# Kernel optimization log

Measured on AMD Instinct MI355X. Metric: run time of the kernel, lower is better.

## Reference

```python
import jax, jax.numpy as jnp
import numpy as np

RADIUS = 1.0
NSAMPLE = 32


def _query_ball(new_xyz, xyz, radius, nsample):
    # new_xyz (B,M,3), xyz (B,N,3) -> idx (B,M,nsample) int32
    B, M, _ = new_xyz.shape
    N = xyz.shape[1]
    # squared distances via ||q||^2 + ||p||^2 - 2 q.p (avoids BxMxNx3 diff tensor)
    q2 = jnp.sum(new_xyz * new_xyz, axis=-1)          # (B,M)
    p2 = jnp.sum(xyz * xyz, axis=-1)                  # (B,N)
    qp = jnp.einsum('bmd,bnd->bmn', new_xyz, xyz)     # (B,M,N)
    dist2 = q2[:, :, None] + p2[:, None, :] - 2.0 * qp
    mask = dist2 < radius * radius
    ar = jnp.arange(N, dtype=jnp.int32)
    masked = jnp.where(mask, ar[None, None, :], jnp.int32(N + 1))  # (B,M,N)
    first = jnp.sort(masked, axis=2)[:, :, :nsample]               # (B,M,S)
    first_valid = first[:, :, :1]                                   # pad with first neighbor
    idx = jnp.where(first == N + 1, first_valid, first)
    return idx.astype(jnp.int32)


def _group(points, idx):
    # points (B,C,N), idx (B,M,S) -> (B,C,M,S) gather along N
    B, C, N = points.shape
    M, S = idx.shape[1], idx.shape[2]
    ie = jnp.broadcast_to(idx.reshape(B, 1, M * S).astype(jnp.int32), (B, C, M * S))
    return jnp.take_along_axis(points, ie, axis=2).reshape(B, C, M, S)


def setup_inputs() -> dict:
    key = jax.random.key(0)
    k1, k2 = jax.random.split(key)
    B, N, M, C = 8, 8192, 2048, 64
    xyz = jax.random.normal(k1, (B, N, 3), dtype=jnp.float32)
    # centroids are a subset of the cloud -> every ball query has >= 1 valid neighbor
    new_xyz = xyz[:, :M, :]
    features = jax.random.normal(k2, (B, C, N), dtype=jnp.float32)
    return {"xyz": xyz, "new_xyz": new_xyz, "features": features}


def reference(xyz, new_xyz, features):
    idx = _query_ball(new_xyz, xyz, RADIUS, NSAMPLE)                      # (B,M,S)
    grouped_xyz = _group(jnp.swapaxes(xyz, 1, 2), idx)                    # (B,3,M,S)
    grouped_xyz = grouped_xyz - jnp.swapaxes(new_xyz, 1, 2)[..., None]    # recenter
    grouped_feat = _group(features, idx)                                  # (B,C,M,S)
    return jnp.concatenate([grouped_xyz, grouped_feat], axis=1)           # (B,3+C,M,S)
```

## Files before the change

### kernel.cpp

```cpp
#include <hip/hip_runtime.h>

#define N_PTS 8192
#define M_Q   2048
#define C_F   64
#define NS    32
#define B_SZ  8

typedef float f32x4 __attribute__((ext_vector_type(4)));

__global__ __launch_bounds__(256) void prep_kernel(
    const float* __restrict__ feat, const float* __restrict__ xyz,
    float* __restrict__ featT, float4* __restrict__ xyz4)
{
#pragma clang fp contract(off)
    __shared__ float lds[C_F * 65];
    if (blockIdx.x < B_SZ * 128) {
        const int b  = blockIdx.x >> 7;
        const int n0 = (blockIdx.x & 127) * 64;
        {
            const int c_lo = (int)threadIdx.x >> 4;
            const int n4   = ((int)threadIdx.x & 15) * 4;
#pragma unroll
            for (int k = 0; k < 4; ++k) {
                const int c = k * 16 + c_lo;
                const float4 v =
                    *(const float4*)&feat[((size_t)b * C_F + c) * N_PTS + n0 + n4];
                lds[c * 65 + n4 + 0] = v.x;
                lds[c * 65 + n4 + 1] = v.y;
                lds[c * 65 + n4 + 2] = v.z;
                lds[c * 65 + n4 + 3] = v.w;
            }
        }
        __syncthreads();
        {
            const int n_lo = (int)threadIdx.x >> 4;
            const int c0   = ((int)threadIdx.x & 15) * 4;
#pragma unroll
            for (int k = 0; k < 4; ++k) {
                const int nn = k * 16 + n_lo;
                float4 w;
                w.x = lds[(c0 + 0) * 65 + nn];
                w.y = lds[(c0 + 1) * 65 + nn];
                w.z = lds[(c0 + 2) * 65 + nn];
                w.w = lds[(c0 + 3) * 65 + nn];
                *(float4*)&featT[((size_t)b * N_PTS + n0 + nn) * C_F + c0] = w;
            }
        }
    } else {
        const int i = (blockIdx.x - B_SZ * 128) * 256 + (int)threadIdx.x;
        const float p0 = xyz[i * 3 + 0];
        const float p1 = xyz[i * 3 + 1];
        const float p2 = xyz[i * 3 + 2];
        const float s  = (p0 * p0 + p1 * p1) + p2 * p2;
        xyz4[i] = make_float4(p0, p1, p2, s);
    }
}

__global__ __launch_bounds__(256) void qbg_kernel(
    const float4* __restrict__ xyz4, const float* __restrict__ nxyz,
    const float* __restrict__ featT, float* __restrict__ out)
{
#pragma clang fp contract(off)
    __shared__ int   sidx[4][NS];
    __shared__ float stage[67 * 33];

    const int lane = threadIdx.x & 63;
    const int w    = threadIdx.x >> 6;
    const int q    = blockIdx.x * 4 + w;
    const int b    = q >> 11;
    const float4* __restrict__ xb = xyz4 + (size_t)b * N_PTS;

    {
        const float* __restrict__ qp = nxyz + (size_t)q * 3;
        const float qx = qp[0], qy = qp[1], qz = qp[2];
        const float q2 = (qx * qx + qy * qy) + qz * qz;

        int  cnt = 0;
        int  first_idx = 0;
        bool have_first = false;

        float4 P[4], Q[4];
#pragma unroll
        for (int cc = 0; cc < 4; ++cc) P[cc] = xb[cc * 64 + lane];

        for (int base = 0; base < N_PTS && cnt < NS; base += 256) {
            const int nb = base + 256;
            if (nb < N_PTS) {
#pragma unroll
                for (int cc = 0; cc < 4; ++cc) Q[cc] = xb[nb + cc * 64 + lane];
            }
#pragma unroll
            for (int cc = 0; cc < 4; ++cc) {
                if (cnt >= NS) break;
                const float qpdot = (qx * P[cc].x + qy * P[cc].y) + qz * P[cc].z;
                const float d2 = (q2 + P[cc].w) - 2.0f * qpdot;
                const bool pred = d2 < 1.0f;
                const unsigned long long mask = __ballot(pred);
                if (mask) {
                    if (!have_first) {
                        first_idx = base + cc * 64 + __ffsll(mask) - 1;
                        have_first = true;
                    }
                    if (pred) {
                        const int pos = cnt + (int)__popcll(mask & ((1ull << lane) - 1ull));
                        if (pos < NS) sidx[w][pos] = base + cc * 64 + lane;
                    }
                    cnt += (int)__popcll(mask);
                }
            }
#pragma unroll
            for (int cc = 0; cc < 4; ++cc) P[cc] = Q[cc];
        }
        if (cnt < NS) {
            for (int p = cnt + lane; p < NS; p += 64) sidx[w][p] = first_idx;
        }
    }
    __syncthreads();

    const int pS = threadIdx.x >> 3;
    const int j  = threadIdx.x & 7;
    const size_t cstride = (size_t)M_Q * NS;

    float4 va, vb, pv;
    float q0v = 0.f, q1v = 0.f, q2v = 0.f;
    {
        const int n0 = sidx[0][pS];
        const float* __restrict__ fb = featT + ((size_t)b * N_PTS + n0) * C_F;
        va = *(const float4*)(fb + j * 4);
        vb = *(const float4*)(fb + 32 + j * 4);
        if (j == 0) {
            pv = xb[n0];
            const float* __restrict__ qp2 = nxyz + (size_t)(blockIdx.x * 4) * 3;
            q0v = qp2[0]; q1v = qp2[1]; q2v = qp2[2];
        }
    }

    for (int w2 = 0; w2 < 4; ++w2) {
        const int ca = j * 4;
        stage[(3 + ca + 0)  * 33 + pS] = va.x;
        stage[(3 + ca + 1)  * 33 + pS] = va.y;
        stage[(3 + ca + 2)  * 33 + pS] = va.z;
        stage[(3 + ca + 3)  * 33 + pS] = va.w;
        stage[(35 + ca + 0) * 33 + pS] = vb.x;
        stage[(35 + ca + 1) * 33 + pS] = vb.y;
        stage[(35 + ca + 2) * 33 + pS] = vb.z;
        stage[(35 + ca + 3) * 33 + pS] = vb.w;
        if (j == 0) {
            stage[0 * 33 + pS] = pv.x - q0v;
            stage[1 * 33 + pS] = pv.y - q1v;
            stage[2 * 33 + pS] = pv.z - q2v;
        }

        float4 van, vbn, pvn;
        float q0n = 0.f, q1n = 0.f, q2n = 0.f;
        if (w2 < 3) {
            const int nx = sidx[w2 + 1][pS];
            const float* __restrict__ fb = featT + ((size_t)b * N_PTS + nx) * C_F;
            van = *(const float4*)(fb + j * 4);
            vbn = *(const float4*)(fb + 32 + j * 4);
            if (j == 0) {
                pvn = xb[nx];
                const float* __restrict__ qp2 =
                    nxyz + (size_t)(blockIdx.x * 4 + w2 + 1) * 3;
                q0n = qp2[0]; q1n = qp2[1]; q2n = qp2[2];
            }
        }
        __syncthreads();

        const int qq = blockIdx.x * 4 + w2;
        const int mm = qq & (M_Q - 1);
        const size_t obase = ((size_t)b * 67 * M_Q + mm) * NS;
#pragma unroll
        for (int it = 0; it < 3; ++it) {
            const int e = it * 256 + (int)threadIdx.x;
            if (e < 67 * 8) {
                const int row  = e >> 3;
                const int col4 = (e & 7) * 4;
                f32x4 v;
                v.x = stage[row * 33 + col4 + 0];
                v.y = stage[row * 33 + col4 + 1];
                v.z = stage[row * 33 + col4 + 2];
                v.w = stage[row * 33 + col4 + 3];
                __builtin_nontemporal_store(
                    v, (f32x4*)&out[obase + (size_t)row * cstride + col4]);
            }
        }
        __syncthreads();

        va = van; vb = vbn; pv = pvn;
        q0v = q0n; q1v = q1n; q2v = q2n;
    }
}

extern "C" void kernel_launch(void* const* d_in, const int* in_sizes, int n_in,
                              void* d_out, int out_size, void* d_ws, size_t ws_size,
                              hipStream_t stream)
{
    const float* xyz  = (const float*)d_in[0];
    const float* nxyz = (const float*)d_in[1];
    const float* feat = (const float*)d_in[2];
    float* out = (float*)d_out;

    float*  featT = (float*)d_ws;
    float4* xyz4  = (float4*)((char*)d_ws + (20 << 20));

    const int Q = B_SZ * M_Q;

    prep_kernel<<<B_SZ * 128 + (B_SZ * N_PTS) / 256, 256, 0, stream>>>(
        feat, xyz, featT, xyz4);
    qbg_kernel<<<Q / 4, 256, 0, stream>>>(xyz4, nxyz, featT, out);
}
```

Baseline: 184.2 us.

## Gather all four queries' neighbors per wave into one staging tile

Each wave now gathers the features and recentered xyz for its own query right after the ball search. They go into a shared staging tile sized for all four queries (67 x 128 columns, padded to 132). The block then writes the whole tile in one pass with 16-byte LDS reads and nontemporal stores covering 512 contiguous bytes per output row. This removes the serialized four-step loop with its eight block barriers and scalar LDS reads. The cost is a larger LDS footprint, about 35 KB, which may lower occupancy, and the loss of the software prefetch of the next query's gather.

```diff
diff --git a/kernel.cpp b/kernel.cpp
--- a/kernel.cpp
+++ b/kernel.cpp
@@ -62,7 +62,7 @@
 {
 #pragma clang fp contract(off)
     __shared__ int   sidx[4][NS];
-    __shared__ float stage[67 * 33];
+    __shared__ float stage[67 * 132];
 
     const int lane = threadIdx.x & 63;
     const int w    = threadIdx.x >> 6;
@@ -70,9 +70,10 @@
     const int b    = q >> 11;
     const float4* __restrict__ xb = xyz4 + (size_t)b * N_PTS;
 
+    const float* __restrict__ qp = nxyz + (size_t)q * 3;
+    const float qx = qp[0], qy = qp[1], qz = qp[2];
+
     {
-        const float* __restrict__ qp = nxyz + (size_t)q * 3;
-        const float qx = qp[0], qy = qp[1], qz = qp[2];
         const float q2 = (qx * qx + qy * qy) + qz * qz;
 
         int  cnt = 0;
@@ -115,80 +116,50 @@
             for (int p = cnt + lane; p < NS; p += 64) sidx[w][p] = first_idx;
         }
     }
+
+    {
+        const int sj = lane & 7;
+        const int sa = lane >> 3;
+#pragma unroll
+        for (int it = 0; it < 4; ++it) {
+            const int s  = it * 8 + sa;
+            const int n  = sidx[w][s];
+            const int col = w * NS + s;
+            const float* __restrict__ fb = featT + ((size_t)b * N_PTS + n) * C_F;
+            const float4 va = *(const float4*)(fb + sj * 4);
+            const float4 vb = *(const float4*)(fb + 32 + sj * 4);
+            const int ca = sj * 4;
+            stage[(3 + ca + 0)  * 132 + col] = va.x;
+            stage[(3 + ca + 1)  * 132 + col] = va.y;
+            stage[(3 + ca + 2)  * 132 + col] = va.z;
+            stage[(3 + ca + 3)  * 132 + col] = va.w;
+            stage[(35 + ca + 0) * 132 + col] = vb.x;
+            stage[(35 + ca + 1) * 132 + col] = vb.y;
+            stage[(35 + ca + 2) * 132 + col] = vb.z;
+            stage[(35 + ca + 3) * 132 + col] = vb.w;
+            if (sj == 0) {
+                const float4 pv = xb[n];
+                stage[0 * 132 + col] = pv.x - qx;
+                stage[1 * 132 + col] = pv.y - qy;
+                stage[2 * 132 + col] = pv.z - qz;
+            }
+        }
+    }
     __syncthreads();
 
-    const int pS = threadIdx.x >> 3;
-    const int j  = threadIdx.x & 7;
+    const int mm0 = (blockIdx.x * 4) & (M_Q - 1);
     const size_t cstride = (size_t)M_Q * NS;
-
-    float4 va, vb, pv;
-    float q0v = 0.f, q1v = 0.f, q2v = 0.f;
-    {
-        const int n0 = sidx[0][pS];
-        const float* __restrict__ fb = featT + ((size_t)b * N_PTS + n0) * C_F;
-        va = *(const float4*)(fb + j * 4);
-        vb = *(const float4*)(fb + 32 + j * 4);
-        if (j == 0) {
-            pv = xb[n0];
-            const float* __restrict__ qp2 = nxyz + (size_t)(blockIdx.x * 4) * 3;
-            q0v = qp2[0]; q1v = qp2[1]; q2v = qp2[2];
+    float* __restrict__ op = out + ((size_t)b * 67 * M_Q + mm0) * NS;
+#pragma unroll
+    for (int it = 0; it < 9; ++it) {
+        const int e = it * 256 + (int)threadIdx.x;
+        if (e < 67 * 32) {
+            const int row = e >> 5;
+            const int c4  = e & 31;
+            const f32x4 v = *(const f32x4*)&stage[row * 132 + c4 * 4];
+            __builtin_nontemporal_store(
+                v, (f32x4*)&op[(size_t)row * cstride + c4 * 4]);
         }
-    }
-
-    for (int w2 = 0; w2 < 4; ++w2) {
-        const int ca = j * 4;
-        stage[(3 + ca + 0)  * 33 + pS] = va.x;
-        stage[(3 + ca + 1)  * 33 + pS] = va.y;
-        stage[(3 + ca + 2)  * 33 + pS] = va.z;
-        stage[(3 + ca + 3)  * 33 + pS] = va.w;
-        stage[(35 + ca + 0) * 33 + pS] = vb.x;
-        stage[(35 + ca + 1) * 33 + pS] = vb.y;
-        stage[(35 + ca + 2) * 33 + pS] = vb.z;
-        stage[(35 + ca + 3) * 33 + pS] = vb.w;
-        if (j == 0) {
-            stage[0 * 33 + pS] = pv.x - q0v;
-            stage[1 * 33 + pS] = pv.y - q1v;
-            stage[2 * 33 + pS] = pv.z - q2v;
-        }
-
-        float4 van, vbn, pvn;
-        float q0n = 0.f, q1n = 0.f, q2n = 0.f;
-        if (w2 < 3) {
-            const int nx = sidx[w2 + 1][pS];
-            const float* __restrict__ fb = featT + ((size_t)b * N_PTS + nx) * C_F;
-            van = *(const float4*)(fb + j * 4);
-            vbn = *(const float4*)(fb + 32 + j * 4);
-            if (j == 0) {
-                pvn = xb[nx];
-                const float* __restrict__ qp2 =
-                    nxyz + (size_t)(blockIdx.x * 4 + w2 + 1) * 3;
-                q0n = qp2[0]; q1n = qp2[1]; q2n = qp2[2];
-            }
-        }
-        __syncthreads();
-
-        const int qq = blockIdx.x * 4 + w2;
-        const int mm = qq & (M_Q - 1);
-        const size_t obase = ((size_t)b * 67 * M_Q + mm) * NS;
-#pragma unroll
-        for (int it = 0; it < 3; ++it) {
-            const int e = it * 256 + (int)threadIdx.x;
-            if (e < 67 * 8) {
-                const int row  = e >> 3;
-                const int col4 = (e & 7) * 4;
-                f32x4 v;
-                v.x = stage[row * 33 + col4 + 0];
-                v.y = stage[row * 33 + col4 + 1];
-                v.z = stage[row * 33 + col4 + 2];
-                v.w = stage[row * 33 + col4 + 3];
-                __builtin_nontemporal_store(
-                    v, (f32x4*)&out[obase + (size_t)row * cstride + col4]);
-            }
-        }
-        __syncthreads();
-
-        va = van; vb = vbn; pv = pvn;
-        q0v = q0n; q1v = q1n; q2v = q2n;
     }
 }
 
```

After: 193.2 us. 1.05x slower.
